# Optimization experiments

Hardware: AMD Instinct MI355X
Metric: run time of the kernel (lower is better)

## Reference

```python
import jax, jax.numpy as jnp
import numpy as np

B, D = 16, 8192
CH = 32
N_BLOCKS = 24
DILATIONS = [2 ** i for i in range(8)] * 3  # 3 stacks of 8 layers


def _causal_conv(x, W, b, dilation):
    # x: (B, Cin, L); W: (Cout, Cin, K). Causal = left-pad (K-1)*dilation only,
    # which equals torch's symmetric-pad-then-slice-right trick.
    pad = (W.shape[-1] - 1) * dilation
    y = jax.lax.conv_general_dilated(
        x, W, window_strides=(1,), padding=[(pad, 0)],
        rhs_dilation=(dilation,), dimension_numbers=('NCH', 'OIH', 'NCH'))
    return y + b[None, :, None]


def setup_inputs() -> dict:
    key = jax.random.key(0)
    ks = jax.random.split(key, 13)
    s = 0.1  # keep activations in a sane range
    return {
        'x': jax.random.normal(ks[0], (B, D), jnp.float32),
        'W0': jax.random.normal(ks[1], (CH, 1, 2), jnp.float32) * s,
        'b0': jax.random.normal(ks[2], (CH,), jnp.float32) * s,
        'Wd': jax.random.normal(ks[3], (N_BLOCKS, 2 * CH, CH, 2), jnp.float32) * s,
        'bd': jax.random.normal(ks[4], (N_BLOCKS, 2 * CH), jnp.float32) * s,
        'W1': jax.random.normal(ks[5], (N_BLOCKS, CH, CH), jnp.float32) * s,
        'b1': jax.random.normal(ks[6], (N_BLOCKS, CH), jnp.float32) * s,
        'Wf': jax.random.normal(ks[7], (CH, CH), jnp.float32) * s,
        'bf': jax.random.normal(ks[8], (CH,), jnp.float32) * s,
        'fW1': jax.random.normal(ks[9], (64, CH * 4), jnp.float32) * s,
        'fb1': jax.random.normal(ks[10], (64,), jnp.float32) * s,
        'fW2': jax.random.normal(ks[11], (10, 64), jnp.float32) * s,
        'fb2': jax.random.normal(ks[12], (10,), jnp.float32) * s,
    }


def reference(x, W0, b0, Wd, bd, W1, b1, Wf, bf, fW1, fb1, fW2, fb2):
    h = _causal_conv(x[:, None, :], W0, b0, 1)  # (B, 32, L)
    skip_sum = jnp.zeros_like(h)
    for i, dil in enumerate(DILATIONS):
        z = _causal_conv(h, Wd[i], bd[i], dil)          # (B, 64, L)
        f, g = jnp.split(z, 2, axis=1)
        gated = jnp.tanh(f) * jax.nn.sigmoid(g)          # (B, 32, L)
        skip = jnp.einsum('oc,bcl->bol', W1[i], gated) + b1[i][None, :, None]
        h = h + skip                                     # residual (dropout = eval identity)
        skip_sum = skip_sum + skip                       # sum of stacked skips
    y = jax.nn.relu(skip_sum)
    y = jnp.einsum('oc,bcl->bol', Wf, y) + bf[None, :, None]
    y = jax.nn.relu(y)
    # AdaptiveMaxPool1d(4): L divisible by 4 -> max over contiguous chunks
    Bc, C, L = y.shape
    y = y.reshape(Bc, C, 4, L // 4).max(axis=-1)         # (B, 32, 4)
    y = y.reshape(Bc, C * 4)
    y = jax.nn.relu(y @ fW1.T + fb1)
    return y @ fW2.T + fb2
```

## Files before the change

kernel.cpp:

```cpp
#include <hip/hip_runtime.h>

#define BATCH 16
#define SEQ 8192
#define CH 32
#define NB 24

typedef __attribute__((ext_vector_type(8))) short short8;
typedef __attribute__((ext_vector_type(4))) short short4v;
typedef __attribute__((ext_vector_type(4))) float f32x4;

__device__ __forceinline__ unsigned short f2bf(float x) {
    unsigned int u = __float_as_uint(x);
    unsigned int r = (u + 0x7FFFu + ((u >> 16) & 1u)) >> 16;
    return (unsigned short)r;
}
__device__ __forceinline__ float bf2f(unsigned short h) {
    return __uint_as_float(((unsigned int)h) << 16);
}

__device__ __forceinline__ float rcp_fast(float x) { return __builtin_amdgcn_rcpf(x); }

__device__ __forceinline__ float fast_tanh(float x) {
    float ax = fabsf(x);
    float e = __expf(-2.0f * ax);
    float t = (1.0f - e) * rcp_fast(1.0f + e);
    return copysignf(t, x);
}
__device__ __forceinline__ float fast_sigmoid(float x) {
    return rcp_fast(1.0f + __expf(-x));
}

__global__ __launch_bounds__(64) void k_prep(const float* __restrict__ Wd,
                                             const float* __restrict__ bd,
                                             const float* __restrict__ W1,
                                             const float* __restrict__ b1,
                                             unsigned short* __restrict__ stream) {
    int i = blockIdx.x;
    int l = threadIdx.x;
    int p = l & 15, h4 = l >> 4;
    const float* wd  = Wd + (size_t)i * 64 * 64;
    const float* w1  = W1 + (size_t)i * 1024;
    const float* bdp = bd + (size_t)i * 64;
    const float* b1p = b1 + (size_t)i * 32;
    unsigned short* out = stream + (size_t)i * (28672 / 2);

    for (int rt = 0; rt < 4; ++rt)
        for (int q = 0; q < 2; ++q) {
            int slot = rt * 2 + q;
            for (int j = 0; j < 8; ++j) {
                int m = 16 * rt + p;
                int k = 32 * q + 8 * h4 + j;
                int c = k & 31, tap = k >> 5;
                float w = wd[m * 64 + c * 2 + tap];
                unsigned short hi = f2bf(w);
                out[(size_t)slot * 512 + l * 8 + j] = hi;
                out[(size_t)(8 + slot) * 512 + l * 8 + j] = f2bf(w - bf2f(hi));
            }
        }
    for (int rt2 = 0; rt2 < 2; ++rt2)
        for (int j = 0; j < 8; ++j) {
            int o = 16 * rt2 + p, c = 8 * h4 + j;
            float w = w1[o * 32 + c];
            unsigned short hi = f2bf(w);
            out[(size_t)(16 + rt2) * 512 + l * 8 + j] = hi;
            out[(size_t)(18 + rt2) * 512 + l * 8 + j] = f2bf(w - bf2f(hi));
        }
    float* outf = (float*)stream + (size_t)i * (28672 / 4);
    for (int rt = 0; rt < 4; ++rt)
        for (int r = 0; r < 4; ++r)
            outf[(size_t)(20 + rt) * 256 + l * 4 + r] = bdp[16 * rt + 4 * h4 + r];
    for (int rt2 = 0; rt2 < 2; ++rt2)
        for (int r = 0; r < 4; ++r)
            outf[(size_t)(24 + rt2) * 256 + l * 4 + r] = b1p[16 * rt2 + 4 * h4 + r];
}

__global__ __launch_bounds__(256) void k_init(const float* __restrict__ x,
                                              const float* __restrict__ W0,
                                              const float* __restrict__ b0,
                                              unsigned short* __restrict__ hhi,
                                              unsigned short* __restrict__ hlo,
                                              float* __restrict__ pooled) {
    int idx = blockIdx.x * 256 + threadIdx.x;
    int b = idx >> 13, t = idx & (SEQ - 1);
    float xt = x[b * SEQ + t];
    float xm = (t > 0) ? x[b * SEQ + t - 1] : 0.0f;
    __align__(16) unsigned short hi[CH], lo[CH];
#pragma unroll
    for (int c = 0; c < CH; ++c) {
        float v = W0[c * 2] * xm + W0[c * 2 + 1] * xt + b0[c];
        hi[c] = f2bf(v);
        lo[c] = f2bf(v - bf2f(hi[c]));
    }
    size_t base = (size_t)idx * CH;
#pragma unroll
    for (int k = 0; k < 4; ++k) {
        *(short8*)(hhi + base + 8 * k) = *(const short8*)(hi + 8 * k);
        *(short8*)(hlo + base + 8 * k) = *(const short8*)(lo + 8 * k);
    }
    if (idx < BATCH * CH * 4) pooled[idx] = 0.0f;
}

__global__ __launch_bounds__(512, 2) void k_stack(
        const unsigned short* __restrict__ in_hi,
        const unsigned short* __restrict__ in_lo,
        unsigned short* __restrict__ out_hi,
        unsigned short* __restrict__ out_lo,
        const unsigned short* __restrict__ wstream,
        int stack) {
    __shared__ __align__(16) unsigned short lhi[768 * 40];
    __shared__ __align__(16) unsigned short llo[768 * 40];
    __shared__ __align__(16) unsigned short gbuf[8][2][16][40];

    int tid = threadIdx.x;
    int lane = tid & 63, wave = tid >> 6;
    int p = lane & 15, h4 = lane >> 4;
    int bb = blockIdx.x >> 4;
    int T0 = (blockIdx.x & 15) * 512;

    const unsigned short* pin_hi = in_hi + (size_t)bb * SEQ * CH;
    const unsigned short* pin_lo = in_lo + (size_t)bb * SEQ * CH;
    unsigned short* pout_hi = out_hi + (size_t)bb * SEQ * CH;
    unsigned short* pout_lo = out_lo + (size_t)bb * SEQ * CH;

    const short8 zero8 = {0, 0, 0, 0, 0, 0, 0, 0};

    for (int i = tid; i < 768; i += 512) {
        int t = T0 - 256 + i;
        if (t >= 0) {
#pragma unroll
            for (int k = 0; k < 4; ++k) {
                *(short8*)&lhi[i * 40 + 8 * k] = *(const short8*)(pin_hi + (size_t)t * CH + 8 * k);
                *(short8*)&llo[i * 40 + 8 * k] = *(const short8*)(pin_lo + (size_t)t * CH + 8 * k);
            }
        } else {
#pragma unroll
            for (int k = 0; k < 4; ++k) {
                *(short8*)&lhi[i * 40 + 8 * k] = zero8;
                *(short8*)&llo[i * 40 + 8 * k] = zero8;
            }
        }
    }
    __syncthreads();

#pragma unroll 1
    for (int l = 0; l < 8; ++l) {
        int dil = 1 << l;
        const unsigned short* frag = wstream + (size_t)(8 * stack + l) * 14336;
        const short8* fs = (const short8*)frag;
        short8 Ah[4][2], Al[4][2], Sh[2], Sl[2];
#pragma unroll
        for (int rt = 0; rt < 4; ++rt)
#pragma unroll
            for (int q = 0; q < 2; ++q) {
                Ah[rt][q] = fs[(rt * 2 + q) * 64 + lane];
                Al[rt][q] = fs[(8 + rt * 2 + q) * 64 + lane];
            }
#pragma unroll
        for (int rt2 = 0; rt2 < 2; ++rt2) {
            Sh[rt2] = fs[(16 + rt2) * 64 + lane];
            Sl[rt2] = fs[(18 + rt2) * 64 + lane];
        }
        const f32x4* ff = (const f32x4*)frag;
        f32x4 bFG[4], bS[2];
#pragma unroll
        for (int rt = 0; rt < 4; ++rt) bFG[rt] = ff[(20 + rt) * 64 + lane];
#pragma unroll
        for (int rt2 = 0; rt2 < 2; ++rt2) bS[rt2] = ff[(24 + rt2) * 64 + lane];

        float hnew[6][2][4];

#pragma unroll
        for (int s6 = 0; s6 < 6; ++s6) {
            int tpos = wave * 96 + s6 * 16 + p;
            int tq = tpos - dil;
            bool ok = (T0 - 256 + tq >= 0);
            int tqc = (tq > 0) ? tq : 0;

            short8 bh1 = *(const short8*)&lhi[tpos * 40 + 8 * h4];
            short8 bl1 = *(const short8*)&llo[tpos * 40 + 8 * h4];
            short8 bh0 = *(const short8*)&lhi[tqc * 40 + 8 * h4];
            short8 bl0 = *(const short8*)&llo[tqc * 40 + 8 * h4];
            if (!ok) { bh0 = zero8; bl0 = zero8; }

            f32x4 acc[4];
#pragma unroll
            for (int rt = 0; rt < 4; ++rt) {
                f32x4 a = bFG[rt];
                a = __builtin_amdgcn_mfma_f32_16x16x32_bf16(Ah[rt][0], bh0, a, 0, 0, 0);
                a = __builtin_amdgcn_mfma_f32_16x16x32_bf16(Ah[rt][1], bh1, a, 0, 0, 0);
                a = __builtin_amdgcn_mfma_f32_16x16x32_bf16(Ah[rt][0], bl0, a, 0, 0, 0);
                a = __builtin_amdgcn_mfma_f32_16x16x32_bf16(Ah[rt][1], bl1, a, 0, 0, 0);
                a = __builtin_amdgcn_mfma_f32_16x16x32_bf16(Al[rt][0], bh0, a, 0, 0, 0);
                a = __builtin_amdgcn_mfma_f32_16x16x32_bf16(Al[rt][1], bh1, a, 0, 0, 0);
                acc[rt] = a;
            }

#pragma unroll
            for (int rt = 0; rt < 2; ++rt) {
                __align__(8) unsigned short g4h[4], g4l[4];
#pragma unroll
                for (int r = 0; r < 4; ++r) {
                    float f = acc[rt][r], g = acc[rt + 2][r];
                    float gated = fast_tanh(f) * fast_sigmoid(g);
                    unsigned short hh = f2bf(gated);
                    g4h[r] = hh;
                    g4l[r] = f2bf(gated - bf2f(hh));
                }
                *(short4v*)&gbuf[wave][0][p][16 * rt + 4 * h4] = *(const short4v*)g4h;
                *(short4v*)&gbuf[wave][1][p][16 * rt + 4 * h4] = *(const short4v*)g4l;
            }
            asm volatile("s_waitcnt lgkmcnt(0)" ::: "memory");
            __builtin_amdgcn_sched_barrier(0);
            short8 Bgh = *(const short8*)&gbuf[wave][0][p][8 * h4];
            short8 Bgl = *(const short8*)&gbuf[wave][1][p][8 * h4];

            f32x4 sacc[2];
#pragma unroll
            for (int rt2 = 0; rt2 < 2; ++rt2) {
                f32x4 a = bS[rt2];
                a = __builtin_amdgcn_mfma_f32_16x16x32_bf16(Sh[rt2], Bgh, a, 0, 0, 0);
                a = __builtin_amdgcn_mfma_f32_16x16x32_bf16(Sh[rt2], Bgl, a, 0, 0, 0);
                a = __builtin_amdgcn_mfma_f32_16x16x32_bf16(Sl[rt2], Bgh, a, 0, 0, 0);
                sacc[rt2] = a;
            }

#pragma unroll
            for (int rt2 = 0; rt2 < 2; ++rt2) {
                int ch = 16 * rt2 + 4 * h4;
                short4v hh = *(const short4v*)&lhi[tpos * 40 + ch];
                short4v hl = *(const short4v*)&llo[tpos * 40 + ch];
#pragma unroll
                for (int r = 0; r < 4; ++r)
                    hnew[s6][rt2][r] = bf2f((unsigned short)hh[r]) +
                                       bf2f((unsigned short)hl[r]) + sacc[rt2][r];
            }
        }
        __syncthreads();

#pragma unroll
        for (int s6 = 0; s6 < 6; ++s6) {
            int tpos = wave * 96 + s6 * 16 + p;
#pragma unroll
            for (int rt2 = 0; rt2 < 2; ++rt2) {
                __align__(8) unsigned short oh[4], ol[4];
#pragma unroll
                for (int r = 0; r < 4; ++r) {
                    float v = hnew[s6][rt2][r];
                    unsigned short nh = f2bf(v);
                    oh[r] = nh;
                    ol[r] = f2bf(v - bf2f(nh));
                }
                int ch = 16 * rt2 + 4 * h4;
                *(short4v*)&lhi[tpos * 40 + ch] = *(const short4v*)oh;
                *(short4v*)&llo[tpos * 40 + ch] = *(const short4v*)ol;
            }
        }
        __syncthreads();
    }

    {
        int i = 256 + tid;
        int t = T0 + tid;
#pragma unroll
        for (int k = 0; k < 4; ++k) {
            *(short8*)(pout_hi + (size_t)t * CH + 8 * k) = *(const short8*)&lhi[i * 40 + 8 * k];
            *(short8*)(pout_lo + (size_t)t * CH + 8 * k) = *(const short8*)&llo[i * 40 + 8 * k];
        }
    }
}

__global__ __launch_bounds__(256) void k_final1(
        const unsigned short* __restrict__ hf_hi,
        const unsigned short* __restrict__ hf_lo,
        const float* __restrict__ x,
        const float* __restrict__ W0,
        const float* __restrict__ b0,
        const float* __restrict__ Wf,
        const float* __restrict__ bf,
        float* __restrict__ pooled) {
    int blk = blockIdx.x;
    int b = blk >> 5;
    int chunk = blk & 31;
    int q = chunk >> 3;
    int t = chunk * 256 + threadIdx.x;

    float xt = x[b * SEQ + t];
    float xm = (t > 0) ? x[b * SEQ + t - 1] : 0.0f;
    const unsigned short* ph = hf_hi + ((size_t)b * SEQ + t) * CH;
    const unsigned short* pl = hf_lo + ((size_t)b * SEQ + t) * CH;
    short8 vh[4], vl[4];
#pragma unroll
    for (int k = 0; k < 4; ++k) {
        vh[k] = *(const short8*)(ph + 8 * k);
        vl[k] = *(const short8*)(pl + 8 * k);
    }
    float r[CH];
#pragma unroll
    for (int k = 0; k < 4; ++k)
#pragma unroll
        for (int j = 0; j < 8; ++j) {
            int c = 8 * k + j;
            float h0 = W0[c * 2] * xm + W0[c * 2 + 1] * xt + b0[c];
            float hf = bf2f((unsigned short)vh[k][j]) + bf2f((unsigned short)vl[k][j]);
            r[c] = fmaxf(hf - h0, 0.0f);
        }

    float y[CH];
#pragma unroll 1
    for (int o = 0; o < CH; ++o) {
        const float* w = Wf + o * CH;
        float a0 = bf[o], a1 = 0.0f, a2 = 0.0f, a3 = 0.0f;
#pragma unroll
        for (int c = 0; c < CH; c += 4) {
            a0 += w[c + 0] * r[c + 0];
            a1 += w[c + 1] * r[c + 1];
            a2 += w[c + 2] * r[c + 2];
            a3 += w[c + 3] * r[c + 3];
        }
        y[o] = fmaxf((a0 + a1) + (a2 + a3), 0.0f);
    }

#pragma unroll
    for (int o = 0; o < CH; ++o) {
#pragma unroll
        for (int off = 32; off >= 1; off >>= 1)
            y[o] = fmaxf(y[o], __shfl_xor(y[o], off));
    }

    __shared__ float red[4 * CH];
    int wave = threadIdx.x >> 6, lane = threadIdx.x & 63;
    if (lane == 0) {
#pragma unroll
        for (int o = 0; o < CH; ++o) red[wave * CH + o] = y[o];
    }
    __syncthreads();
    if (threadIdx.x < CH) {
        float m = fmaxf(fmaxf(red[threadIdx.x], red[CH + threadIdx.x]),
                        fmaxf(red[2 * CH + threadIdx.x], red[3 * CH + threadIdx.x]));
        atomicMax((unsigned int*)&pooled[b * (CH * 4) + threadIdx.x * 4 + q],
                  __float_as_uint(m));
    }
}

__global__ __launch_bounds__(1024) void k_final2(const float* __restrict__ pooled,
                                                 const float* __restrict__ fW1,
                                                 const float* __restrict__ fb1,
                                                 const float* __restrict__ fW2,
                                                 const float* __restrict__ fb2,
                                                 float* __restrict__ out) {
    __shared__ float y1[BATCH * 64];
    int tid = threadIdx.x;
    int b = tid >> 6, o = tid & 63;
    float acc = fb1[o];
#pragma unroll
    for (int j = 0; j < 128; ++j) acc += fW1[o * 128 + j] * pooled[b * 128 + j];
    y1[b * 64 + o] = fmaxf(acc, 0.0f);
    __syncthreads();
    if (tid < BATCH * 10) {
        int bb = tid / 10, o2 = tid % 10;
        float a2 = fb2[o2];
#pragma unroll
        for (int j = 0; j < 64; ++j) a2 += fW2[o2 * 64 + j] * y1[bb * 64 + j];
        out[bb * 10 + o2] = a2;
    }
}

extern "C" void kernel_launch(void* const* d_in, const int* in_sizes, int n_in,
                              void* d_out, int out_size, void* d_ws, size_t ws_size,
                              hipStream_t stream) {
    const float* x   = (const float*)d_in[0];
    const float* W0  = (const float*)d_in[1];
    const float* b0  = (const float*)d_in[2];
    const float* Wd  = (const float*)d_in[3];
    const float* bd  = (const float*)d_in[4];
    const float* W1  = (const float*)d_in[5];
    const float* b1  = (const float*)d_in[6];
    const float* Wf  = (const float*)d_in[7];
    const float* bf  = (const float*)d_in[8];
    const float* fW1 = (const float*)d_in[9];
    const float* fb1 = (const float*)d_in[10];
    const float* fW2 = (const float*)d_in[11];
    const float* fb2 = (const float*)d_in[12];
    float* out = (float*)d_out;

    const size_t HS = (size_t)BATCH * SEQ * CH;
    unsigned short* Ahi = (unsigned short*)d_ws;
    unsigned short* Alo = Ahi + HS;
    unsigned short* Bhi = Alo + HS;
    unsigned short* Blo = Bhi + HS;
    unsigned short* wstream = Blo + HS;
    float* pooled = (float*)(wstream + (size_t)NB * 14336);

    k_prep<<<NB, 64, 0, stream>>>(Wd, bd, W1, b1, wstream);
    k_init<<<512, 256, 0, stream>>>(x, W0, b0, Ahi, Alo, pooled);

    k_stack<<<256, 512, 0, stream>>>(Ahi, Alo, Bhi, Blo, wstream, 0);
    k_stack<<<256, 512, 0, stream>>>(Bhi, Blo, Ahi, Alo, wstream, 1);
    k_stack<<<256, 512, 0, stream>>>(Ahi, Alo, Bhi, Blo, wstream, 2);

    k_final1<<<512, 256, 0, stream>>>(Bhi, Blo, x, W0, b0, Wf, bf, pooled);
    k_final2<<<1, 1024, 0, stream>>>(pooled, fW1, fb1, fW2, fb2, out);
}
```

Baseline: 392.8 us.

## Store hidden state as fp32 in LDS and global, split to bf16 on load

```diff
diff --git a/kernel.cpp b/kernel.cpp
--- a/kernel.cpp
+++ b/kernel.cpp
@@ -1,4 +1,5 @@
 #include <hip/hip_runtime.h>
+#include <hip/hip_bf16.h>
 
 #define BATCH 16
 #define SEQ 8192
@@ -9,25 +10,30 @@
 typedef __attribute__((ext_vector_type(4))) short short4v;
 typedef __attribute__((ext_vector_type(4))) float f32x4;
 
+#define LROW 36
+
 __device__ __forceinline__ unsigned short f2bf(float x) {
-    unsigned int u = __float_as_uint(x);
-    unsigned int r = (u + 0x7FFFu + ((u >> 16) & 1u)) >> 16;
-    return (unsigned short)r;
+    __hip_bfloat16 b = __float2bfloat16(x);
+    unsigned short u;
+    __builtin_memcpy(&u, &b, 2);
+    return u;
 }
 __device__ __forceinline__ float bf2f(unsigned short h) {
     return __uint_as_float(((unsigned int)h) << 16);
 }
-
 __device__ __forceinline__ float rcp_fast(float x) { return __builtin_amdgcn_rcpf(x); }
 
-__device__ __forceinline__ float fast_tanh(float x) {
-    float ax = fabsf(x);
-    float e = __expf(-2.0f * ax);
-    float t = (1.0f - e) * rcp_fast(1.0f + e);
-    return copysignf(t, x);
-}
-__device__ __forceinline__ float fast_sigmoid(float x) {
-    return rcp_fast(1.0f + __expf(-x));
+__device__ __forceinline__ float gate_fn(float f, float g) {
+    float ef = __expf(-2.0f * fabsf(f));
+    float eg = __expf(-g);
+    float num = 1.0f - ef;
+    float den = (1.0f + ef) * (1.0f + eg);
+    return copysignf(num * rcp_fast(den), f);
+}
+
+__device__ __forceinline__ void split2(float v, unsigned short& h, unsigned short& l) {
+    h = f2bf(v);
+    l = f2bf(v - bf2f(h));
 }
 
 __global__ __launch_bounds__(64) void k_prep(const float* __restrict__ Wd,
@@ -77,38 +83,29 @@
 __global__ __launch_bounds__(256) void k_init(const float* __restrict__ x,
                                               const float* __restrict__ W0,
                                               const float* __restrict__ b0,
-                                              unsigned short* __restrict__ hhi,
-                                              unsigned short* __restrict__ hlo,
+                                              float* __restrict__ h,
                                               float* __restrict__ pooled) {
     int idx = blockIdx.x * 256 + threadIdx.x;
     int b = idx >> 13, t = idx & (SEQ - 1);
     float xt = x[b * SEQ + t];
     float xm = (t > 0) ? x[b * SEQ + t - 1] : 0.0f;
-    __align__(16) unsigned short hi[CH], lo[CH];
-#pragma unroll
-    for (int c = 0; c < CH; ++c) {
-        float v = W0[c * 2] * xm + W0[c * 2 + 1] * xt + b0[c];
-        hi[c] = f2bf(v);
-        lo[c] = f2bf(v - bf2f(hi[c]));
-    }
-    size_t base = (size_t)idx * CH;
-#pragma unroll
-    for (int k = 0; k < 4; ++k) {
-        *(short8*)(hhi + base + 8 * k) = *(const short8*)(hi + 8 * k);
-        *(short8*)(hlo + base + 8 * k) = *(const short8*)(lo + 8 * k);
-    }
+    __align__(16) float hv[CH];
+#pragma unroll
+    for (int c = 0; c < CH; ++c)
+        hv[c] = W0[c * 2] * xm + W0[c * 2 + 1] * xt + b0[c];
+    float* dst = h + (size_t)idx * CH;
+#pragma unroll
+    for (int k = 0; k < 8; ++k)
+        *(f32x4*)(dst + 4 * k) = *(const f32x4*)(hv + 4 * k);
     if (idx < BATCH * CH * 4) pooled[idx] = 0.0f;
 }
 
 __global__ __launch_bounds__(512, 2) void k_stack(
-        const unsigned short* __restrict__ in_hi,
-        const unsigned short* __restrict__ in_lo,
-        unsigned short* __restrict__ out_hi,
-        unsigned short* __restrict__ out_lo,
+        const float* __restrict__ hin,
+        float* __restrict__ hout,
         const unsigned short* __restrict__ wstream,
         int stack) {
-    __shared__ __align__(16) unsigned short lhi[768 * 40];
-    __shared__ __align__(16) unsigned short llo[768 * 40];
+    __shared__ __align__(16) float lh[768 * LROW];
     __shared__ __align__(16) unsigned short gbuf[8][2][16][40];
 
     int tid = threadIdx.x;
@@ -117,27 +114,23 @@
     int bb = blockIdx.x >> 4;
     int T0 = (blockIdx.x & 15) * 512;
 
-    const unsigned short* pin_hi = in_hi + (size_t)bb * SEQ * CH;
-    const unsigned short* pin_lo = in_lo + (size_t)bb * SEQ * CH;
-    unsigned short* pout_hi = out_hi + (size_t)bb * SEQ * CH;
-    unsigned short* pout_lo = out_lo + (size_t)bb * SEQ * CH;
-
-    const short8 zero8 = {0, 0, 0, 0, 0, 0, 0, 0};
+    const float* pin = hin + (size_t)bb * SEQ * CH;
+    float* pout = hout + (size_t)bb * SEQ * CH;
+
+    const f32x4 zero4 = {0.0f, 0.0f, 0.0f, 0.0f};
 
     for (int i = tid; i < 768; i += 512) {
         int t = T0 - 256 + i;
+        float* dst = &lh[i * LROW];
         if (t >= 0) {
-#pragma unroll
-            for (int k = 0; k < 4; ++k) {
-                *(short8*)&lhi[i * 40 + 8 * k] = *(const short8*)(pin_hi + (size_t)t * CH + 8 * k);
-                *(short8*)&llo[i * 40 + 8 * k] = *(const short8*)(pin_lo + (size_t)t * CH + 8 * k);
-            }
+            const float* src = pin + (size_t)t * CH;
+#pragma unroll
+            for (int k = 0; k < 8; ++k)
+                *(f32x4*)(dst + 4 * k) = *(const f32x4*)(src + 4 * k);
         } else {
 #pragma unroll
-            for (int k = 0; k < 4; ++k) {
-                *(short8*)&lhi[i * 40 + 8 * k] = zero8;
-                *(short8*)&llo[i * 40 + 8 * k] = zero8;
-            }
+            for (int k = 0; k < 8; ++k)
+                *(f32x4*)(dst + 4 * k) = zero4;
         }
     }
     __syncthreads();
@@ -167,7 +160,7 @@
 #pragma unroll
         for (int rt2 = 0; rt2 < 2; ++rt2) bS[rt2] = ff[(24 + rt2) * 64 + lane];
 
-        float hnew[6][2][4];
+        f32x4 hnew[6][2];
 
 #pragma unroll
         for (int s6 = 0; s6 < 6; ++s6) {
@@ -176,11 +169,20 @@
             bool ok = (T0 - 256 + tq >= 0);
             int tqc = (tq > 0) ? tq : 0;
 
-            short8 bh1 = *(const short8*)&lhi[tpos * 40 + 8 * h4];
-            short8 bl1 = *(const short8*)&llo[tpos * 40 + 8 * h4];
-            short8 bh0 = *(const short8*)&lhi[tqc * 40 + 8 * h4];
-            short8 bl0 = *(const short8*)&llo[tqc * 40 + 8 * h4];
-            if (!ok) { bh0 = zero8; bl0 = zero8; }
+            const float* r1 = &lh[tpos * LROW + 8 * h4];
+            const float* r0 = &lh[tqc * LROW + 8 * h4];
+            f32x4 v1a = *(const f32x4*)r1, v1b = *(const f32x4*)(r1 + 4);
+            f32x4 v0a = *(const f32x4*)r0, v0b = *(const f32x4*)(r0 + 4);
+            if (!ok) { v0a = zero4; v0b = zero4; }
+            short8 bh1, bl1, bh0, bl0;
+#pragma unroll
+            for (int j = 0; j < 4; ++j) {
+                unsigned short hh, ll;
+                split2(v1a[j], hh, ll); bh1[j] = (short)hh; bl1[j] = (short)ll;
+                split2(v1b[j], hh, ll); bh1[4 + j] = (short)hh; bl1[4 + j] = (short)ll;
+                split2(v0a[j], hh, ll); bh0[j] = (short)hh; bl0[j] = (short)ll;
+                split2(v0b[j], hh, ll); bh0[4 + j] = (short)hh; bl0[4 + j] = (short)ll;
+            }
 
             f32x4 acc[4];
 #pragma unroll
@@ -200,11 +202,8 @@
                 __align__(8) unsigned short g4h[4], g4l[4];
 #pragma unroll
                 for (int r = 0; r < 4; ++r) {
-                    float f = acc[rt][r], g = acc[rt + 2][r];
-                    float gated = fast_tanh(f) * fast_sigmoid(g);
-                    unsigned short hh = f2bf(gated);
-                    g4h[r] = hh;
-                    g4l[r] = f2bf(gated - bf2f(hh));
+                    float gated = gate_fn(acc[rt][r], acc[rt + 2][r]);
+                    split2(gated, g4h[r], g4l[r]);
                 }
                 *(short4v*)&gbuf[wave][0][p][16 * rt + 4 * h4] = *(const short4v*)g4h;
                 *(short4v*)&gbuf[wave][1][p][16 * rt + 4 * h4] = *(const short4v*)g4l;
@@ -226,13 +225,8 @@
 
 #pragma unroll
             for (int rt2 = 0; rt2 < 2; ++rt2) {
-                int ch = 16 * rt2 + 4 * h4;
-                short4v hh = *(const short4v*)&lhi[tpos * 40 + ch];
-                short4v hl = *(const short4v*)&llo[tpos * 40 + ch];
-#pragma unroll
-                for (int r = 0; r < 4; ++r)
-                    hnew[s6][rt2][r] = bf2f((unsigned short)hh[r]) +
-                                       bf2f((unsigned short)hl[r]) + sacc[rt2][r];
+                f32x4 hold = *(const f32x4*)&lh[tpos * LROW + 16 * rt2 + 4 * h4];
+                hnew[s6][rt2] = hold + sacc[rt2];
             }
         }
         __syncthreads();
@@ -241,19 +235,8 @@
         for (int s6 = 0; s6 < 6; ++s6) {
             int tpos = wave * 96 + s6 * 16 + p;
 #pragma unroll
-            for (int rt2 = 0; rt2 < 2; ++rt2) {
-                __align__(8) unsigned short oh[4], ol[4];
-#pragma unroll
-                for (int r = 0; r < 4; ++r) {
-                    float v = hnew[s6][rt2][r];
-                    unsigned short nh = f2bf(v);
-                    oh[r] = nh;
-                    ol[r] = f2bf(v - bf2f(nh));
-                }
-                int ch = 16 * rt2 + 4 * h4;
-                *(short4v*)&lhi[tpos * 40 + ch] = *(const short4v*)oh;
-                *(short4v*)&llo[tpos * 40 + ch] = *(const short4v*)ol;
-            }
+            for (int rt2 = 0; rt2 < 2; ++rt2)
+                *(f32x4*)&lh[tpos * LROW + 16 * rt2 + 4 * h4] = hnew[s6][rt2];
         }
         __syncthreads();
     }
@@ -261,17 +244,16 @@
     {
         int i = 256 + tid;
         int t = T0 + tid;
-#pragma unroll
-        for (int k = 0; k < 4; ++k) {
-            *(short8*)(pout_hi + (size_t)t * CH + 8 * k) = *(const short8*)&lhi[i * 40 + 8 * k];
-            *(short8*)(pout_lo + (size_t)t * CH + 8 * k) = *(const short8*)&llo[i * 40 + 8 * k];
-        }
+        const float* src = &lh[i * LROW];
+        float* dst = pout + (size_t)t * CH;
+#pragma unroll
+        for (int k = 0; k < 8; ++k)
+            *(f32x4*)(dst + 4 * k) = *(const f32x4*)(src + 4 * k);
     }
 }
 
 __global__ __launch_bounds__(256) void k_final1(
-        const unsigned short* __restrict__ hf_hi,
-        const unsigned short* __restrict__ hf_lo,
+        const float* __restrict__ hfin,
         const float* __restrict__ x,
         const float* __restrict__ W0,
         const float* __restrict__ b0,
@@ -286,23 +268,19 @@
 
     float xt = x[b * SEQ + t];
     float xm = (t > 0) ? x[b * SEQ + t - 1] : 0.0f;
-    const unsigned short* ph = hf_hi + ((size_t)b * SEQ + t) * CH;
-    const unsigned short* pl = hf_lo + ((size_t)b * SEQ + t) * CH;
-    short8 vh[4], vl[4];
-#pragma unroll
-    for (int k = 0; k < 4; ++k) {
-        vh[k] = *(const short8*)(ph + 8 * k);
-        vl[k] = *(const short8*)(pl + 8 * k);
-    }
+    const float* ph = hfin + ((size_t)b * SEQ + t) * CH;
+    f32x4 v[8];
+#pragma unroll
+    for (int k = 0; k < 8; ++k) v[k] = *(const f32x4*)(ph + 4 * k);
+
     float r[CH];
 #pragma unroll
-    for (int k = 0; k < 4; ++k)
-#pragma unroll
-        for (int j = 0; j < 8; ++j) {
-            int c = 8 * k + j;
+    for (int k = 0; k < 8; ++k)
+#pragma unroll
+        for (int j = 0; j < 4; ++j) {
+            int c = 4 * k + j;
             float h0 = W0[c * 2] * xm + W0[c * 2 + 1] * xt + b0[c];
-            float hf = bf2f((unsigned short)vh[k][j]) + bf2f((unsigned short)vl[k][j]);
-            r[c] = fmaxf(hf - h0, 0.0f);
+            r[c] = fmaxf(v[k][j] - h0, 0.0f);
         }
 
     float y[CH];
@@ -384,20 +362,18 @@
     float* out = (float*)d_out;
 
     const size_t HS = (size_t)BATCH * SEQ * CH;
-    unsigned short* Ahi = (unsigned short*)d_ws;
-    unsigned short* Alo = Ahi + HS;
-    unsigned short* Bhi = Alo + HS;
-    unsigned short* Blo = Bhi + HS;
-    unsigned short* wstream = Blo + HS;
+    float* bufA = (float*)d_ws;
+    float* bufB = bufA + HS;
+    unsigned short* wstream = (unsigned short*)(bufB + HS);
     float* pooled = (float*)(wstream + (size_t)NB * 14336);
 
     k_prep<<<NB, 64, 0, stream>>>(Wd, bd, W1, b1, wstream);
-    k_init<<<512, 256, 0, stream>>>(x, W0, b0, Ahi, Alo, pooled);
-
-    k_stack<<<256, 512, 0, stream>>>(Ahi, Alo, Bhi, Blo, wstream, 0);
-    k_stack<<<256, 512, 0, stream>>>(Bhi, Blo, Ahi, Alo, wstream, 1);
-    k_stack<<<256, 512, 0, stream>>>(Ahi, Alo, Bhi, Blo, wstream, 2);
-
-    k_final1<<<512, 256, 0, stream>>>(Bhi, Blo, x, W0, b0, Wf, bf, pooled);
+    k_init<<<512, 256, 0, stream>>>(x, W0, b0, bufA, pooled);
+
+    k_stack<<<256, 512, 0, stream>>>(bufA, bufB, wstream, 0);
+    k_stack<<<256, 512, 0, stream>>>(bufB, bufA, wstream, 1);
+    k_stack<<<256, 512, 0, stream>>>(bufA, bufB, wstream, 2);
+
+    k_final1<<<512, 256, 0, stream>>>(bufB, x, W0, b0, Wf, bf, pooled);
     k_final2<<<1, 1024, 0, stream>>>(pooled, fW1, fb1, fW2, fb2, out);
 }
```

New measurement: 365.7 us. 1.07x faster.
